# Kernel optimization log

Hardware: AMD Instinct MI355X
Metric: run time of the kernel (lower is better)

Reference implementation:

```python
import jax, jax.numpy as jnp
import numpy as np
from jax import lax

EPS = 1e-5
B, T, H, L, K = 64, 1024, 12, 120, 5  # batch, seq len, hidden, lstm layers, conv kernel


def _init(key, shape, scale):
    return scale * jax.random.normal(key, shape, dtype=jnp.float32)


def setup_inputs() -> dict:
    key = jax.random.key(0)
    ks = jax.random.split(key, 16)
    return {
        "x": jax.random.normal(ks[0], (B, 6, T), dtype=jnp.float32),
        "conv_acc_w": _init(ks[1], (6, 6, K), 0.3),
        "conv_acc_b": jnp.zeros((6,), jnp.float32),
        "bn1_gamma": jnp.ones((6,), jnp.float32),
        "bn1_beta": jnp.zeros((6,), jnp.float32),
        "conv_ang_w": _init(ks[2], (6, 6, K), 0.3),
        "conv_ang_b": jnp.zeros((6,), jnp.float32),
        "bn2_gamma": jnp.ones((6,), jnp.float32),
        "bn2_beta": jnp.zeros((6,), jnp.float32),
        "attn_w": _init(ks[3], (H, 6), 0.4),
        "attn_b": jnp.zeros((H,), jnp.float32),
        "lstm_wih": _init(ks[4], (L, 4 * H, H), 0.2),
        "lstm_whh": _init(ks[5], (L, 4 * H, H), 0.2),
        "lstm_bih": _init(ks[6], (L, 4 * H), 0.1),
        "lstm_bhh": _init(ks[7], (L, 4 * H), 0.1),
        "lin1_w": _init(ks[8], (H, H), 0.3),
        "lin1_b": jnp.zeros((H,), jnp.float32),
        "lin2_w": _init(ks[9], (H, H), 0.3),
        "lin2_b": jnp.zeros((H,), jnp.float32),
        "mu_w": _init(ks[10], (H, H), 0.3),
        "mu_b": jnp.zeros((H,), jnp.float32),
        "sigma_w": _init(ks[11], (H, H), 0.3),
        "sigma_b": jnp.zeros((H,), jnp.float32),
    }


def _conv1d(x, w, b):
    # x: (B, C, T) valid conv, matches nn.Conv1d
    y = lax.conv_general_dilated(x, w, (1,), "VALID", dimension_numbers=("NCH", "OIH", "NCH"))
    return y + b[None, :, None]


def _batchnorm(x, gamma, beta):
    # training-mode BatchNorm1d: biased batch stats over (N, T)
    mean = jnp.mean(x, axis=(0, 2), keepdims=True)
    var = jnp.var(x, axis=(0, 2), keepdims=True)
    return (x - mean) * lax.rsqrt(var + EPS) * gamma[None, :, None] + beta[None, :, None]


def _lstm_stack(seq_tbh, wih, whh, bias):
    # seq_tbh: (T', B, H); stacked 120-layer LSTM, torch gate order (i, f, g, o)
    b = seq_tbh.shape[1]
    h0 = jnp.zeros((b, H), seq_tbh.dtype)

    def layer(seq, p):
        w_ih, w_hh, bb = p

        def step(carry, xt):
            h, c = carry
            g = xt @ w_ih.T + h @ w_hh.T + bb  # (B, 4H)
            i, f, gg, o = jnp.split(g, 4, axis=-1)
            c_new = jax.nn.sigmoid(f) * c + jax.nn.sigmoid(i) * jnp.tanh(gg)
            h_new = jax.nn.sigmoid(o) * jnp.tanh(c_new)
            return (h_new, c_new), h_new

        (h_T, _), out = lax.scan(step, (h0, h0), seq)
        return out, h_T

    _, h_last = lax.scan(layer, seq_tbh, (wih, whh, bias))
    return h_last  # (L, B, H): final hidden state of every layer


def _forward(x, conv_acc_w, conv_acc_b, bn1_gamma, bn1_beta, conv_ang_w, conv_ang_b,
             bn2_gamma, bn2_beta, attn_w, attn_b, lstm_wih, lstm_whh, lstm_bih, lstm_bhh,
             lin1_w, lin1_b, lin2_w, lin2_b, mu_w, mu_b, sigma_w, sigma_b):
    out_acc = jax.nn.relu(_batchnorm(_conv1d(x, conv_acc_w, conv_acc_b), bn1_gamma, bn1_beta))
    out_ang = jax.nn.relu(_batchnorm(_conv1d(out_acc, conv_ang_w, conv_ang_b), bn2_gamma, bn2_beta))
    feat = jax.nn.relu(jnp.einsum("bct,hc->bth", out_ang, attn_w) + attn_b)  # (B, T-8, H)
    seq = jnp.transpose(feat, (1, 0, 2))  # (T', B, H) time-major for scan
    h_last = _lstm_stack(seq, lstm_wih, lstm_whh, lstm_bih + lstm_bhh)
    h = jnp.transpose(h_last, (1, 0, 2))  # (B, L, H) == hidden_state.permute(1,0,2)
    h = jax.nn.relu(h @ lin1_w.T + lin1_b)
    out = jax.nn.relu(h @ lin2_w.T + lin2_b)
    mu = out @ mu_w.T + mu_b
    log_var = jax.nn.softplus(out @ sigma_w.T + sigma_b)
    return out, mu, log_var


def reference(x, conv_acc_w, conv_acc_b, bn1_gamma, bn1_beta, conv_ang_w, conv_ang_b,
              bn2_gamma, bn2_beta, attn_w, attn_b, lstm_wih, lstm_whh, lstm_bih, lstm_bhh,
              lin1_w, lin1_b, lin2_w, lin2_b, mu_w, mu_b, sigma_w, sigma_b):
    return _forward(x, conv_acc_w, conv_acc_b, bn1_gamma, bn1_beta, conv_ang_w, conv_ang_b,
                    bn2_gamma, bn2_beta, attn_w, attn_b, lstm_wih, lstm_whh, lstm_bih, lstm_bhh,
                    lin1_w, lin1_b, lin2_w, lin2_b, mu_w, mu_b, sigma_w, sigma_b)
```

## Files before the change

### kernel.cpp

```cpp
#include <hip/hip_runtime.h>
#include <math.h>

#define NLAY 120
#define TT   1016
#define NB   64
#define RB   8
#define IRS  32
#define TPB  384
#define BIGF (1 << 20)

typedef float v2f __attribute__((ext_vector_type(2)));

__device__ __forceinline__ float fast_rcp(float x) { return __builtin_amdgcn_rcpf(x); }
__device__ __forceinline__ float fast_sig(float x) { return fast_rcp(1.f + __expf(-x)); }
__device__ __forceinline__ float fast_tanh(float x) { return 1.f - 2.f * fast_rcp(1.f + __expf(2.f * x)); }

__device__ __forceinline__ int poll_ge_ag(const int* p, int tgt, int cur) {
  long g = 0;
  while (cur < tgt) {
    cur = __hip_atomic_load(p, __ATOMIC_RELAXED, __HIP_MEMORY_SCOPE_AGENT);
    if (cur >= tgt) break;
    __builtin_amdgcn_s_sleep(1);
    if (++g > 400000L) break;
  }
  return cur;
}
__device__ __forceinline__ int poll_ge_wg(const int* p, int tgt, int cur) {
  long g = 0;
  while (cur < tgt) {
    cur = __hip_atomic_load(p, __ATOMIC_RELAXED, __HIP_MEMORY_SCOPE_WORKGROUP);
    if (cur >= tgt) break;
    __builtin_amdgcn_s_sleep(1);
    if (++g > 400000L) break;
  }
  return cur;
}

__global__ void k_conv(const float* __restrict__ xin, const float* __restrict__ cw,
                       const float* __restrict__ cb, const float* __restrict__ aff,
                       float* __restrict__ yout, float* __restrict__ stat,
                       int Tin, int Tout, int use_aff)
{
  const int bx = blockIdx.x;
  const int b = bx / 6, co = bx - b * 6;
  const int tid = threadIdx.x;
  __shared__ float wsh[30];
  __shared__ float ssh[6], shsh[6];
  if (tid < 30) wsh[tid] = cw[co * 30 + tid];
  if (tid < 6) {
    ssh[tid]  = use_aff ? aff[tid] : 1.f;
    shsh[tid] = use_aff ? aff[6 + tid] : 0.f;
  }
  __syncthreads();
  const float bias = cb[co];
  float lsum = 0.f, lsq = 0.f;
  for (int t = tid; t < Tout; t += 256) {
    float acc = bias;
#pragma unroll
    for (int ci = 0; ci < 6; ++ci) {
      const float* xr = xin + ((size_t)b * 6 + ci) * Tin + t;
      const float s = ssh[ci], sh = shsh[ci];
#pragma unroll
      for (int k = 0; k < 5; ++k) {
        float v = xr[k];
        if (use_aff) v = fmaxf(fmaf(s, v, sh), 0.f);
        acc += wsh[ci * 5 + k] * v;
      }
    }
    yout[((size_t)b * 6 + co) * Tout + t] = acc;
    lsum += acc; lsq += acc * acc;
  }
  __shared__ float rs[256], rq[256];
  rs[tid] = lsum; rq[tid] = lsq;
  __syncthreads();
  for (int s = 128; s > 0; s >>= 1) {
    if (tid < s) { rs[tid] += rs[tid + s]; rq[tid] += rq[tid + s]; }
    __syncthreads();
  }
  if (tid == 0) { atomicAdd(&stat[co], rs[0]); atomicAdd(&stat[6 + co], rq[0]); }
}

__global__ void k_finalize(const float* __restrict__ stat,
                           const float* __restrict__ gamma, const float* __restrict__ beta,
                           float* __restrict__ aff, float invN)
{
  const int c = threadIdx.x;
  if (c < 6) {
    float mean = stat[c] * invN;
    float var  = stat[6 + c] * invN - mean * mean;
    float sc   = gamma[c] * rsqrtf(var + 1e-5f);
    aff[c]     = sc;
    aff[6 + c] = fmaf(-mean, sc, beta[c]);
  }
}

__global__ void k_attn(const float* __restrict__ y2, const float* __restrict__ aff2,
                       const float* __restrict__ aw, const float* __restrict__ ab,
                       float* __restrict__ seq0)
{
  const int t = blockIdx.x;
  const int tid = threadIdx.x;
  __shared__ float zb[6 * 64];
  if (tid < 384) {
    const int c = tid >> 6, bb = tid & 63;
    float v = y2[((size_t)bb * 6 + c) * TT + t];
    zb[c * 64 + bb] = fmaxf(fmaf(aff2[c], v, aff2[6 + c]), 0.f);
  }
  __syncthreads();
  const int b = tid / 12, j = tid - b * 12;
  float acc = ab[j];
#pragma unroll
  for (int c = 0; c < 6; ++c) acc += aw[j * 6 + c] * zb[c * 64 + b];
  seq0[(size_t)t * 768 + tid] = fmaxf(acc, 0.f);
}

__global__ __launch_bounds__(TPB, 2) void k_lstm(
    const float* __restrict__ wih, const float* __restrict__ whh,
    const float* __restrict__ bih, const float* __restrict__ bhh,
    const float* __restrict__ seq0, float* __restrict__ ring,
    int* __restrict__ prog, int* __restrict__ cons,
    float* __restrict__ hfin)
{
  const int bid  = blockIdx.x;
  const int c    = bid >> 2;
  const int seg  = bid & 3;
  const int tid  = threadIdx.x;
  const int w    = tid >> 6;
  const int lane = tid & 63;
  const int p    = lane / 12;
  const int j    = lane - p * 12;
  const bool act = (p < 5);
  const int pc   = act ? p : 0;
  const int l    = seg * 30 + w * 5 + pc;

  __shared__ __align__(16) float hloc[6][2][64];
  __shared__ __align__(16) float iring[5][IRS][12];
  __shared__ __align__(16) float xring[2][16][12];
  __shared__ __align__(16) float oring[16][12];
  __shared__ int pflag[6];
  __shared__ int cflag[8];
  float* xrf = &xring[0][0][0];

  if (tid < 6) pflag[tid] = 0;
  if (tid < 8) cflag[tid] = 0;
  hloc[w][0][lane] = 0.f; hloc[w][1][lane] = 0.f;
  __syncthreads();

  v2f wx_if[12], wx_go[12], wh_if[12], wh_go[12];
  v2f b_if = (v2f){0.f, 0.f}, b_go = (v2f){0.f, 0.f};
  if (act) {
    const float* wi = wih + l * 576;
    const float* wh = whh + l * 576;
#pragma unroll
    for (int k = 0; k < 12; ++k) {
      wx_if[k] = (v2f){ wi[(j     ) * 12 + k], wi[(j + 12) * 12 + k] };
      wx_go[k] = (v2f){ wi[(j + 24) * 12 + k], wi[(j + 36) * 12 + k] };
      wh_if[k] = (v2f){ wh[(j     ) * 12 + k], wh[(j + 12) * 12 + k] };
      wh_go[k] = (v2f){ wh[(j + 24) * 12 + k], wh[(j + 36) * 12 + k] };
    }
    const float* ba = bih + l * 48;
    const float* bb = bhh + l * 48;
    b_if = (v2f){ ba[j]      + bb[j],      ba[j + 12] + bb[j + 12] };
    b_go = (v2f){ ba[j + 24] + bb[j + 24], ba[j + 36] + bb[j + 36] };
  }

  const int hop_in  = c * 3 + seg - 1;
  const int hop_out = c * 3 + seg;
  const float* rin  = ring + (size_t)((seg > 0) ? hop_in : 0) * (RB * 192);
  float*       rout = ring + (size_t)((seg < 3) ? hop_out : 0) * (RB * 192);
  const bool is_feeder = (w == 0);
  const bool is_tailer = (w == 5) && (seg < 3);

  const int f0 = lane, f1 = lane + 64, f2 = lane + 128;
  const int s0o0 = (f0 / 12) * 768 + (f0 % 12);
  const int s0o1 = (f1 / 12) * 768 + (f1 % 12);
  const int s0o2 = (f2 / 12) * 768 + (f2 % 12);

  auto ld_batch = [&](int m, float* d) {
    if (seg == 0) {
      const float* b = seq0 + (size_t)m * 16 * 768 + c * 12;
      d[0] = b[s0o0]; d[1] = b[s0o1]; d[2] = b[s0o2];
    } else {
      const float* b = rin + (m & (RB - 1)) * 192;
      d[0] = __hip_atomic_load(b + f0, __ATOMIC_RELAXED, __HIP_MEMORY_SCOPE_AGENT);
      d[1] = __hip_atomic_load(b + f1, __ATOMIC_RELAXED, __HIP_MEMORY_SCOPE_AGENT);
      d[2] = __hip_atomic_load(b + f2, __ATOMIC_RELAXED, __HIP_MEMORY_SCOPE_AGENT);
    }
  };

  float pend[3] = {0.f, 0.f, 0.f};
  int kp = 0, kcons = 0;
  if (is_feeder) {
    if (seg > 0) kp = poll_ge_ag(&prog[hop_in], 2, 0);
    float cur[3];
    ld_batch(0, cur);
    ld_batch(1, pend);
    xrf[f0] = cur[0]; xrf[f1] = cur[1]; xrf[f2] = cur[2];
  }

  float cst = 0.f;
  int pcache = 0, ccache = 0;

  auto step = [&](int s, bool guard) __attribute__((always_inline)) {
    const int t  = s - pc;
    const int rb = (s & 1) ^ 1, wb = s & 1;

    const float* ax;
    if (p == 0) ax = (w == 0) ? (xrf + ((s >> 4) & 1) * 192 + (s & 15) * 12)
                              : (&iring[w - 1][s & (IRS - 1)][0]);
    else        ax = &hloc[w][rb][(pc == 0 ? 0 : pc - 1) * 12];
    const float* ah = &hloc[w][rb][pc * 12];

    float4 xA = ((const float4*)ax)[0], xB = ((const float4*)ax)[1], xC = ((const float4*)ax)[2];
    float4 hA = ((const float4*)ah)[0], hB = ((const float4*)ah)[1], hC = ((const float4*)ah)[2];
    float xv[12] = {xA.x,xA.y,xA.z,xA.w, xB.x,xB.y,xB.z,xB.w, xC.x,xC.y,xC.z,xC.w};
    float hv[12] = {hA.x,hA.y,hA.z,hA.w, hB.x,hB.y,hB.z,hB.w, hC.x,hC.y,hC.z,hC.w};

    v2f axif = (v2f){0.f,0.f}, axgo = (v2f){0.f,0.f};
    v2f ahif = b_if, ahgo = b_go;
#pragma unroll
    for (int k = 0; k < 12; ++k) {
      v2f xx = { xv[k], xv[k] };
      axif = __builtin_elementwise_fma(wx_if[k], xx, axif);
      axgo = __builtin_elementwise_fma(wx_go[k], xx, axgo);
    }
#pragma unroll
    for (int k = 0; k < 12; ++k) {
      v2f hh = { hv[k], hv[k] };
      ahif = __builtin_elementwise_fma(wh_if[k], hh, ahif);
      ahgo = __builtin_elementwise_fma(wh_go[k], hh, ahgo);
    }
    v2f aif = axif + ahif, ago = axgo + ahgo;
    float ig = fast_sig(aif.x);
    float fg = fast_sig(aif.y);
    float gg = fast_tanh(ago.x);
    float og = fast_sig(ago.y);

    if (!guard) {
      cst = fg * cst + ig * gg;
      float hn = og * fast_tanh(cst);
      hloc[w][wb][p * 12 + j] = hn;
      if (p == 4) {
        if (w < 5) iring[w][t & (IRS - 1)][j] = hn;
        else if (seg < 3) oring[t & 15][j] = hn;
      }
    } else {
      const bool run = act && (t >= 0) && (t < TT);
      if (run) {
        cst = fg * cst + ig * gg;
        float hn = og * fast_tanh(cst);
        hloc[w][wb][p * 12 + j] = hn;
        if (p == 4) {
          if (w < 5) iring[w][t & (IRS - 1)][j] = hn;
          else if (seg < 3) oring[t & 15][j] = hn;
        }
        if (t == TT - 1) hfin[l * 768 + c * 12 + j] = hn;
      }
    }

    if (is_tailer) {
      const int t4 = s - 4;
      if (t4 >= 0 && t4 < TT && (((t4 & 15) == 15) || t4 == TT - 1)) {
        const int m4 = t4 >> 4;
        if (kcons < m4 - (RB - 1) + 1)
          kcons = poll_ge_ag(&cons[hop_out], m4 - RB + 1, kcons);
        const float* orf = &oring[0][0];
        float o0 = orf[f0], o1 = orf[f1], o2 = orf[f2];
        float* d = rout + (m4 & (RB - 1)) * 192;
        __hip_atomic_store(d + f0, o0, __ATOMIC_RELAXED, __HIP_MEMORY_SCOPE_AGENT);
        __hip_atomic_store(d + f1, o1, __ATOMIC_RELAXED, __HIP_MEMORY_SCOPE_AGENT);
        __hip_atomic_store(d + f2, o2, __ATOMIC_RELAXED, __HIP_MEMORY_SCOPE_AGENT);
        if (lane == 0)
          __hip_atomic_store(&prog[hop_out], m4 + 1, __ATOMIC_RELEASE, __HIP_MEMORY_SCOPE_AGENT);
      }
    }
  };

  for (int s4 = 0; s4 < 1024; s4 += 4) {
    if (is_feeder && (s4 & 15) == 0) {
      const int m = s4 >> 4;
      if (m + 1 < NB) {
        float* xd = xrf + ((m + 1) & 1) * 192;
        xd[f0] = pend[0]; xd[f1] = pend[1]; xd[f2] = pend[2];
      }
      if (m + 2 < NB) {
        if (seg > 0 && kp < m + 3) kp = poll_ge_ag(&prog[hop_in], m + 3, kp);
        ld_batch(m + 2, pend);
      }
      if (seg > 0 && lane == 0)
        __hip_atomic_store(&cons[hop_in], m, __ATOMIC_RELAXED, __HIP_MEMORY_SCOPE_AGENT);
    }

    if (w > 0 && s4 < TT) {
      const int tgt = (s4 + 4 < TT) ? (s4 + 4) : TT;
      if (pcache < tgt) {
        pcache = poll_ge_wg(&pflag[w - 1], tgt, pcache);
        asm volatile("" ::: "memory");
      }
    }
    if (w < 5 && s4 >= 36) {
      const int tgt = s4 - 32;
      if (ccache < tgt) {
        ccache = poll_ge_wg(&cflag[w + 1], tgt, ccache);
        asm volatile("" ::: "memory");
      }
    }

    if (s4 >= 4 && s4 < 1012) {
      step(s4 + 0, false); step(s4 + 1, false); step(s4 + 2, false); step(s4 + 3, false);
    } else {
      step(s4 + 0, true);  step(s4 + 1, true);  step(s4 + 2, true);  step(s4 + 3, true);
    }

    if (lane == 0) {
      asm volatile("" ::: "memory");
      if (w < 5)
        __hip_atomic_store(&pflag[w], s4, __ATOMIC_RELAXED, __HIP_MEMORY_SCOPE_WORKGROUP);
      if (w > 0 && s4 + 3 < TT)
        __hip_atomic_store(&cflag[w], s4 + 4, __ATOMIC_RELAXED, __HIP_MEMORY_SCOPE_WORKGROUP);
    }
  }

  if (lane == 0) {
    asm volatile("" ::: "memory");
    if (w < 5) __hip_atomic_store(&pflag[w], BIGF, __ATOMIC_RELAXED, __HIP_MEMORY_SCOPE_WORKGROUP);
    if (w > 0) __hip_atomic_store(&cflag[w], BIGF, __ATOMIC_RELAXED, __HIP_MEMORY_SCOPE_WORKGROUP);
    if (is_feeder && seg > 0)
      __hip_atomic_store(&cons[hop_in], BIGF, __ATOMIC_RELAXED, __HIP_MEMORY_SCOPE_AGENT);
  }
}

__global__ void k_head(const float* __restrict__ hfin,
                       const float* __restrict__ w1, const float* __restrict__ b1,
                       const float* __restrict__ w2, const float* __restrict__ b2,
                       const float* __restrict__ wm, const float* __restrict__ bm,
                       const float* __restrict__ wsg, const float* __restrict__ bsg,
                       float* __restrict__ out)
{
  const int tid = threadIdx.x;
  __shared__ float s1[144], s2[144], sm[144], ss[144];
  __shared__ float v1[12], v2[12], vm[12], vs[12];
  if (tid < 144) { s1[tid] = w1[tid]; s2[tid] = w2[tid]; sm[tid] = wm[tid]; ss[tid] = wsg[tid]; }
  if (tid < 12)  { v1[tid] = b1[tid]; v2[tid] = b2[tid]; vm[tid] = bm[tid]; vs[tid] = bsg[tid]; }
  __syncthreads();
  const int r = blockIdx.x * 256 + tid;
  const int b = r / 120, l = r - b * 120;
  float h[12];
#pragma unroll
  for (int k = 0; k < 12; ++k) h[k] = hfin[l * 768 + b * 12 + k];
  float u1[12];
#pragma unroll
  for (int u = 0; u < 12; ++u) {
    float a = v1[u];
#pragma unroll
    for (int k = 0; k < 12; ++k) a += s1[u * 12 + k] * h[k];
    u1[u] = fmaxf(a, 0.f);
  }
  float u2[12];
#pragma unroll
  for (int u = 0; u < 12; ++u) {
    float a = v2[u];
#pragma unroll
    for (int k = 0; k < 12; ++k) a += s2[u * 12 + k] * u1[k];
    u2[u] = fmaxf(a, 0.f);
  }
  const size_t base = (size_t)r * 12;
#pragma unroll
  for (int u = 0; u < 12; ++u) out[base + u] = u2[u];
#pragma unroll
  for (int u = 0; u < 12; ++u) {
    float a = vm[u];
#pragma unroll
    for (int k = 0; k < 12; ++k) a += sm[u * 12 + k] * u2[k];
    out[92160 + base + u] = a;
  }
#pragma unroll
  for (int u = 0; u < 12; ++u) {
    float a = vs[u];
#pragma unroll
    for (int k = 0; k < 12; ++k) a += ss[u * 12 + k] * u2[k];
    out[184320 + base + u] = fmaxf(a, 0.f) + log1pf(expf(-fabsf(a)));
  }
}

extern "C" void kernel_launch(void* const* d_in, const int* in_sizes, int n_in,
                              void* d_out, int out_size, void* d_ws, size_t ws_size,
                              hipStream_t stream)
{
  const float* x   = (const float*)d_in[0];
  const float* c1w = (const float*)d_in[1];
  const float* c1b = (const float*)d_in[2];
  const float* g1  = (const float*)d_in[3];
  const float* be1 = (const float*)d_in[4];
  const float* c2w = (const float*)d_in[5];
  const float* c2b = (const float*)d_in[6];
  const float* g2  = (const float*)d_in[7];
  const float* be2 = (const float*)d_in[8];
  const float* aw  = (const float*)d_in[9];
  const float* ab  = (const float*)d_in[10];
  const float* wih = (const float*)d_in[11];
  const float* whh = (const float*)d_in[12];
  const float* bih = (const float*)d_in[13];
  const float* bhh = (const float*)d_in[14];
  const float* l1w = (const float*)d_in[15];
  const float* l1b = (const float*)d_in[16];
  const float* l2w = (const float*)d_in[17];
  const float* l2b = (const float*)d_in[18];
  const float* muw = (const float*)d_in[19];
  const float* mub = (const float*)d_in[20];
  const float* sgw = (const float*)d_in[21];
  const float* sgb = (const float*)d_in[22];

  float* ws    = (float*)d_ws;
  float* stat1 = ws;
  float* stat2 = ws + 12;
  float* aff1  = ws + 24;
  float* aff2  = ws + 36;
  int*   prog  = (int*)(ws + 64);
  int*   cons  = (int*)(ws + 304);
  float* y1    = ws + 576;
  float* y2    = y1 + 391680;
  float* seq0  = y2 + 390144;
  float* ring  = seq0 + 780288;
  float* hfin  = ring + (size_t)192 * RB * 192;

  hipMemsetAsync(d_ws, 0, 576 * sizeof(float), stream);

  k_conv<<<384, 256, 0, stream>>>(x, c1w, c1b, nullptr, y1, stat1, 1024, 1020, 0);
  k_finalize<<<1, 64, 0, stream>>>(stat1, g1, be1, aff1, 1.f / 65280.f);
  k_conv<<<384, 256, 0, stream>>>(y1, c2w, c2b, aff1, y2, stat2, 1020, 1016, 1);
  k_finalize<<<1, 64, 0, stream>>>(stat2, g2, be2, aff2, 1.f / 65024.f);
  k_attn<<<1016, 768, 0, stream>>>(y2, aff2, aw, ab, seq0);
  k_lstm<<<256, TPB, 0, stream>>>(wih, whh, bih, bhh, seq0, ring, prog, cons, hfin);
  k_head<<<30, 256, 0, stream>>>(hfin, l1w, l1b, l2w, l2b, muw, mub, sgw, sgb, (float*)d_out);
}
```

Baseline: 812.8 us.

## Exchange LSTM hidden state via ds_bpermute instead of LDS double buffer

Removes the per-wave LDS double buffer for hidden state and instead broadcasts each lane's new h to the next layer lane-group through ds_bpermute cross-lane shuffles, cutting LDS store/load round trips on the serial recurrence path. It also splits the FMA accumulation into two independent chains to shorten dependency latency, switches sigmoid/tanh to raw exp2 intrinsics, drops the s_sleep in the workgroup-scope spin wait, and moves the tailer output flush out of the per-step lambda to once per 4-step block. The risks are more hot spinning on LDS flags and bpermute latency replacing LDS latency.

```diff
diff --git a/kernel.cpp b/kernel.cpp
--- a/kernel.cpp
+++ b/kernel.cpp
@@ -10,10 +10,15 @@
 #define BIGF (1 << 20)
 
 typedef float v2f __attribute__((ext_vector_type(2)));
+typedef float v4f __attribute__((ext_vector_type(4)));
 
 __device__ __forceinline__ float fast_rcp(float x) { return __builtin_amdgcn_rcpf(x); }
-__device__ __forceinline__ float fast_sig(float x) { return fast_rcp(1.f + __expf(-x)); }
-__device__ __forceinline__ float fast_tanh(float x) { return 1.f - 2.f * fast_rcp(1.f + __expf(2.f * x)); }
+__device__ __forceinline__ float sigx(float x) {
+  return fast_rcp(1.f + __builtin_amdgcn_exp2f(-1.442695040888963f * x));
+}
+__device__ __forceinline__ float tanhx(float x) {
+  return 1.f - 2.f * fast_rcp(1.f + __builtin_amdgcn_exp2f(2.885390081777927f * x));
+}
 
 __device__ __forceinline__ int poll_ge_ag(const int* p, int tgt, int cur) {
   long g = 0;
@@ -30,8 +35,7 @@
   while (cur < tgt) {
     cur = __hip_atomic_load(p, __ATOMIC_RELAXED, __HIP_MEMORY_SCOPE_WORKGROUP);
     if (cur >= tgt) break;
-    __builtin_amdgcn_s_sleep(1);
-    if (++g > 400000L) break;
+    if (++g > 3000000L) break;
   }
   return cur;
 }
@@ -131,9 +135,11 @@
   const int j    = lane - p * 12;
   const bool act = (p < 5);
   const int pc   = act ? p : 0;
+  const int pp   = (pc == 0) ? 0 : pc - 1;
   const int l    = seg * 30 + w * 5 + pc;
-
-  __shared__ __align__(16) float hloc[6][2][64];
+  const int base_own = pc * 48;
+  const int base_prv = pp * 48;
+
   __shared__ __align__(16) float iring[5][IRS][12];
   __shared__ __align__(16) float xring[2][16][12];
   __shared__ __align__(16) float oring[16][12];
@@ -143,7 +149,6 @@
 
   if (tid < 6) pflag[tid] = 0;
   if (tid < 8) cflag[tid] = 0;
-  hloc[w][0][lane] = 0.f; hloc[w][1][lane] = 0.f;
   __syncthreads();
 
   v2f wx_if[12], wx_go[12], wh_if[12], wh_go[12];
@@ -198,48 +203,60 @@
     xrf[f0] = cur[0]; xrf[f1] = cur[1]; xrf[f2] = cur[2];
   }
 
-  float cst = 0.f;
+  float hn = 0.f, cst = 0.f;
   int pcache = 0, ccache = 0;
 
   auto step = [&](int s, bool guard) __attribute__((always_inline)) {
     const int t  = s - pc;
-    const int rb = (s & 1) ^ 1, wb = s & 1;
-
-    const float* ax;
-    if (p == 0) ax = (w == 0) ? (xrf + ((s >> 4) & 1) * 192 + (s & 15) * 12)
-                              : (&iring[w - 1][s & (IRS - 1)][0]);
-    else        ax = &hloc[w][rb][(pc == 0 ? 0 : pc - 1) * 12];
-    const float* ah = &hloc[w][rb][pc * 12];
-
-    float4 xA = ((const float4*)ax)[0], xB = ((const float4*)ax)[1], xC = ((const float4*)ax)[2];
-    float4 hA = ((const float4*)ah)[0], hB = ((const float4*)ah)[1], hC = ((const float4*)ah)[2];
-    float xv[12] = {xA.x,xA.y,xA.z,xA.w, xB.x,xB.y,xB.z,xB.w, xC.x,xC.y,xC.z,xC.w};
-    float hv[12] = {hA.x,hA.y,hA.z,hA.w, hB.x,hB.y,hB.z,hB.w, hC.x,hC.y,hC.z,hC.w};
-
-    v2f axif = (v2f){0.f,0.f}, axgo = (v2f){0.f,0.f};
-    v2f ahif = b_if, ahgo = b_go;
-#pragma unroll
-    for (int k = 0; k < 12; ++k) {
-      v2f xx = { xv[k], xv[k] };
-      axif = __builtin_elementwise_fma(wx_if[k], xx, axif);
-      axgo = __builtin_elementwise_fma(wx_go[k], xx, axgo);
-    }
-#pragma unroll
-    for (int k = 0; k < 12; ++k) {
-      v2f hh = { hv[k], hv[k] };
-      ahif = __builtin_elementwise_fma(wh_if[k], hh, ahif);
-      ahgo = __builtin_elementwise_fma(wh_go[k], hh, ahgo);
-    }
-    v2f aif = axif + ahif, ago = axgo + ahgo;
-    float ig = fast_sig(aif.x);
-    float fg = fast_sig(aif.y);
-    float gg = fast_tanh(ago.x);
-    float og = fast_sig(ago.y);
+    const int hb = __float_as_int(hn);
+
+    float hv[12], xv[12];
+#pragma unroll
+    for (int k = 0; k < 12; ++k)
+      hv[k] = __int_as_float(__builtin_amdgcn_ds_bpermute(base_own + 4 * k, hb));
+#pragma unroll
+    for (int k = 0; k < 12; ++k)
+      xv[k] = __int_as_float(__builtin_amdgcn_ds_bpermute(base_prv + 4 * k, hb));
+
+    if (p == 0) {
+      const float* ax = (w == 0) ? (xrf + ((s >> 4) & 1) * 192 + (s & 15) * 12)
+                                 : (&iring[w - 1][s & (IRS - 1)][0]);
+      v4f A = ((const v4f*)ax)[0], Bv = ((const v4f*)ax)[1], C = ((const v4f*)ax)[2];
+      xv[0] = A.x;  xv[1] = A.y;  xv[2]  = A.z;  xv[3]  = A.w;
+      xv[4] = Bv.x; xv[5] = Bv.y; xv[6]  = Bv.z; xv[7]  = Bv.w;
+      xv[8] = C.x;  xv[9] = C.y;  xv[10] = C.z;  xv[11] = C.w;
+    }
+
+    v2f xia = b_if, xib = (v2f){0.f, 0.f};
+    v2f xga = b_go, xgb = (v2f){0.f, 0.f};
+    v2f hia = (v2f){0.f, 0.f}, hib = (v2f){0.f, 0.f};
+    v2f hga = (v2f){0.f, 0.f}, hgb = (v2f){0.f, 0.f};
+#pragma unroll
+    for (int k = 0; k < 6; ++k) {
+      v2f xs = (v2f){ xv[k], xv[k] }, hs = (v2f){ hv[k], hv[k] };
+      xia = __builtin_elementwise_fma(wx_if[k], xs, xia);
+      xga = __builtin_elementwise_fma(wx_go[k], xs, xga);
+      hia = __builtin_elementwise_fma(wh_if[k], hs, hia);
+      hga = __builtin_elementwise_fma(wh_go[k], hs, hga);
+    }
+#pragma unroll
+    for (int k = 6; k < 12; ++k) {
+      v2f xs = (v2f){ xv[k], xv[k] }, hs = (v2f){ hv[k], hv[k] };
+      xib = __builtin_elementwise_fma(wx_if[k], xs, xib);
+      xgb = __builtin_elementwise_fma(wx_go[k], xs, xgb);
+      hib = __builtin_elementwise_fma(wh_if[k], hs, hib);
+      hgb = __builtin_elementwise_fma(wh_go[k], hs, hgb);
+    }
+    v2f aif = (xia + xib) + (hia + hib);
+    v2f ago = (xga + xgb) + (hga + hgb);
+    float ig = sigx(aif.x);
+    float fg = sigx(aif.y);
+    float gg = tanhx(ago.x);
+    float og = sigx(ago.y);
 
     if (!guard) {
       cst = fg * cst + ig * gg;
-      float hn = og * fast_tanh(cst);
-      hloc[w][wb][p * 12 + j] = hn;
+      hn = og * tanhx(cst);
       if (p == 4) {
         if (w < 5) iring[w][t & (IRS - 1)][j] = hn;
         else if (seg < 3) oring[t & 15][j] = hn;
@@ -248,8 +265,7 @@
       const bool run = act && (t >= 0) && (t < TT);
       if (run) {
         cst = fg * cst + ig * gg;
-        float hn = og * fast_tanh(cst);
-        hloc[w][wb][p * 12 + j] = hn;
+        hn = og * tanhx(cst);
         if (p == 4) {
           if (w < 5) iring[w][t & (IRS - 1)][j] = hn;
           else if (seg < 3) oring[t & 15][j] = hn;
@@ -257,11 +273,47 @@
         if (t == TT - 1) hfin[l * 768 + c * 12 + j] = hn;
       }
     }
+  };
+
+  for (int s4 = 0; s4 < 1024; s4 += 4) {
+    if (is_feeder && (s4 & 15) == 0) {
+      const int m = s4 >> 4;
+      if (m + 1 < NB) {
+        float* xd = xrf + ((m + 1) & 1) * 192;
+        xd[f0] = pend[0]; xd[f1] = pend[1]; xd[f2] = pend[2];
+      }
+      if (m + 2 < NB) {
+        if (seg > 0 && kp < m + 3) kp = poll_ge_ag(&prog[hop_in], m + 3, kp);
+        ld_batch(m + 2, pend);
+      }
+      if (seg > 0 && lane == 0)
+        __hip_atomic_store(&cons[hop_in], m, __ATOMIC_RELAXED, __HIP_MEMORY_SCOPE_AGENT);
+    }
+
+    if (w > 0 && s4 < TT) {
+      const int tgt = (s4 + 4 < TT) ? (s4 + 4) : TT;
+      if (pcache < tgt) {
+        pcache = poll_ge_wg(&pflag[w - 1], tgt, pcache);
+        asm volatile("" ::: "memory");
+      }
+    }
+    if (w < 5 && s4 >= 36) {
+      const int tgt = s4 - 32;
+      if (ccache < tgt) {
+        ccache = poll_ge_wg(&cflag[w + 1], tgt, ccache);
+        asm volatile("" ::: "memory");
+      }
+    }
+
+    if (s4 >= 4 && s4 < 1012) {
+      step(s4 + 0, false); step(s4 + 1, false); step(s4 + 2, false); step(s4 + 3, false);
+    } else {
+      step(s4 + 0, true);  step(s4 + 1, true);  step(s4 + 2, true);  step(s4 + 3, true);
+    }
 
     if (is_tailer) {
-      const int t4 = s - 4;
-      if (t4 >= 0 && t4 < TT && (((t4 & 15) == 15) || t4 == TT - 1)) {
-        const int m4 = t4 >> 4;
+      if ((((s4 & 15) == 0) && s4 >= 16) || s4 == 1016) {
+        const int m4 = (s4 - 1) >> 4;
         if (kcons < m4 - (RB - 1) + 1)
           kcons = poll_ge_ag(&cons[hop_out], m4 - RB + 1, kcons);
         const float* orf = &oring[0][0];
@@ -273,43 +325,6 @@
         if (lane == 0)
           __hip_atomic_store(&prog[hop_out], m4 + 1, __ATOMIC_RELEASE, __HIP_MEMORY_SCOPE_AGENT);
       }
-    }
-  };
-
-  for (int s4 = 0; s4 < 1024; s4 += 4) {
-    if (is_feeder && (s4 & 15) == 0) {
-      const int m = s4 >> 4;
-      if (m + 1 < NB) {
-        float* xd = xrf + ((m + 1) & 1) * 192;
-        xd[f0] = pend[0]; xd[f1] = pend[1]; xd[f2] = pend[2];
-      }
-      if (m + 2 < NB) {
-        if (seg > 0 && kp < m + 3) kp = poll_ge_ag(&prog[hop_in], m + 3, kp);
-        ld_batch(m + 2, pend);
-      }
-      if (seg > 0 && lane == 0)
-        __hip_atomic_store(&cons[hop_in], m, __ATOMIC_RELAXED, __HIP_MEMORY_SCOPE_AGENT);
-    }
-
-    if (w > 0 && s4 < TT) {
-      const int tgt = (s4 + 4 < TT) ? (s4 + 4) : TT;
-      if (pcache < tgt) {
-        pcache = poll_ge_wg(&pflag[w - 1], tgt, pcache);
-        asm volatile("" ::: "memory");
-      }
-    }
-    if (w < 5 && s4 >= 36) {
-      const int tgt = s4 - 32;
-      if (ccache < tgt) {
-        ccache = poll_ge_wg(&cflag[w + 1], tgt, ccache);
-        asm volatile("" ::: "memory");
-      }
-    }
-
-    if (s4 >= 4 && s4 < 1012) {
-      step(s4 + 0, false); step(s4 + 1, false); step(s4 + 2, false); step(s4 + 3, false);
-    } else {
-      step(s4 + 0, true);  step(s4 + 1, true);  step(s4 + 2, true);  step(s4 + 3, true);
     }
 
     if (lane == 0) {
```

After: 986.0 us. +21.3%, slower.

## Process two batch columns per LSTM block, halving block count

Applied to the files above, without the earlier changes.

Each LSTM workgroup now carries two batch elements through the layer pipeline instead of one. The per-thread weights held in registers are reused for both columns, and all shared-memory rings and the global hop rings are doubled in width, so the grid shrinks from 256 to 128 blocks. The tailer flush that pushes outputs to the next segment moves out of the per-step lambda into the 4-step loop body, so it is checked once per group of four steps rather than on every step. This gives each wave twice the independent FMA and transcendental work between synchronisation points, at the cost of more register pressure and fewer blocks spread across the CUs.

```diff
diff --git a/kernel.cpp b/kernel.cpp
--- a/kernel.cpp
+++ b/kernel.cpp
@@ -122,7 +122,7 @@
     float* __restrict__ hfin)
 {
   const int bid  = blockIdx.x;
-  const int c    = bid >> 2;
+  const int pr   = bid >> 2;
   const int seg  = bid & 3;
   const int tid  = threadIdx.x;
   const int w    = tid >> 6;
@@ -133,17 +133,20 @@
   const int pc   = act ? p : 0;
   const int l    = seg * 30 + w * 5 + pc;
 
-  __shared__ __align__(16) float hloc[6][2][64];
-  __shared__ __align__(16) float iring[5][IRS][12];
-  __shared__ __align__(16) float xring[2][16][12];
-  __shared__ __align__(16) float oring[16][12];
+  __shared__ __align__(16) float hloc[6][2][2][64];
+  __shared__ __align__(16) float iring[5][IRS][2][12];
+  __shared__ __align__(16) float xring[2][16][2][12];
+  __shared__ __align__(16) float oring[16][2][12];
   __shared__ int pflag[6];
   __shared__ int cflag[8];
-  float* xrf = &xring[0][0][0];
+  float* xrf = &xring[0][0][0][0];
 
   if (tid < 6) pflag[tid] = 0;
   if (tid < 8) cflag[tid] = 0;
-  hloc[w][0][lane] = 0.f; hloc[w][1][lane] = 0.f;
+#pragma unroll
+  for (int z = 0; z < 2; ++z) {
+    hloc[w][0][z][lane] = 0.f; hloc[w][1][z][lane] = 0.f;
+  }
   __syncthreads();
 
   v2f wx_if[12], wx_go[12], wh_if[12], wh_go[12];
@@ -164,114 +167,140 @@
     b_go = (v2f){ ba[j + 24] + bb[j + 24], ba[j + 36] + bb[j + 36] };
   }
 
-  const int hop_in  = c * 3 + seg - 1;
-  const int hop_out = c * 3 + seg;
-  const float* rin  = ring + (size_t)((seg > 0) ? hop_in : 0) * (RB * 192);
-  float*       rout = ring + (size_t)((seg < 3) ? hop_out : 0) * (RB * 192);
+  const int hop_in  = pr * 3 + seg - 1;
+  const int hop_out = pr * 3 + seg;
+  const float* rin  = ring + (size_t)((seg > 0) ? hop_in : 0) * (RB * 384);
+  float*       rout = ring + (size_t)((seg < 3) ? hop_out : 0) * (RB * 384);
   const bool is_feeder = (w == 0);
   const bool is_tailer = (w == 5) && (seg < 3);
 
-  const int f0 = lane, f1 = lane + 64, f2 = lane + 128;
-  const int s0o0 = (f0 / 12) * 768 + (f0 % 12);
-  const int s0o1 = (f1 / 12) * 768 + (f1 % 12);
-  const int s0o2 = (f2 / 12) * 768 + (f2 % 12);
+  int s0o[6];
+#pragma unroll
+  for (int k = 0; k < 6; ++k) {
+    const int fk = lane + 64 * k;
+    const int tl = fk / 24, rem = fk - tl * 24;
+    const int ch = rem / 12, jj = rem - ch * 12;
+    s0o[k] = tl * 768 + ch * 12 + jj;
+  }
 
   auto ld_batch = [&](int m, float* d) {
     if (seg == 0) {
-      const float* b = seq0 + (size_t)m * 16 * 768 + c * 12;
-      d[0] = b[s0o0]; d[1] = b[s0o1]; d[2] = b[s0o2];
+      const float* b = seq0 + (size_t)m * 16 * 768 + pr * 24;
+#pragma unroll
+      for (int k = 0; k < 6; ++k) d[k] = b[s0o[k]];
     } else {
-      const float* b = rin + (m & (RB - 1)) * 192;
-      d[0] = __hip_atomic_load(b + f0, __ATOMIC_RELAXED, __HIP_MEMORY_SCOPE_AGENT);
-      d[1] = __hip_atomic_load(b + f1, __ATOMIC_RELAXED, __HIP_MEMORY_SCOPE_AGENT);
-      d[2] = __hip_atomic_load(b + f2, __ATOMIC_RELAXED, __HIP_MEMORY_SCOPE_AGENT);
+      const float* b = rin + (m & (RB - 1)) * 384;
+#pragma unroll
+      for (int k = 0; k < 6; ++k)
+        d[k] = __hip_atomic_load(b + lane + 64 * k, __ATOMIC_RELAXED, __HIP_MEMORY_SCOPE_AGENT);
     }
   };
 
-  float pend[3] = {0.f, 0.f, 0.f};
+  float pend[6] = {0.f, 0.f, 0.f, 0.f, 0.f, 0.f};
   int kp = 0, kcons = 0;
   if (is_feeder) {
     if (seg > 0) kp = poll_ge_ag(&prog[hop_in], 2, 0);
-    float cur[3];
+    float cur[6];
     ld_batch(0, cur);
     ld_batch(1, pend);
-    xrf[f0] = cur[0]; xrf[f1] = cur[1]; xrf[f2] = cur[2];
-  }
-
-  float cst = 0.f;
+#pragma unroll
+    for (int k = 0; k < 6; ++k) xrf[lane + 64 * k] = cur[k];
+  }
+
+  float cstA = 0.f, cstB = 0.f;
   int pcache = 0, ccache = 0;
 
   auto step = [&](int s, bool guard) __attribute__((always_inline)) {
     const int t  = s - pc;
     const int rb = (s & 1) ^ 1, wb = s & 1;
 
-    const float* ax;
-    if (p == 0) ax = (w == 0) ? (xrf + ((s >> 4) & 1) * 192 + (s & 15) * 12)
-                              : (&iring[w - 1][s & (IRS - 1)][0]);
-    else        ax = &hloc[w][rb][(pc == 0 ? 0 : pc - 1) * 12];
-    const float* ah = &hloc[w][rb][pc * 12];
-
-    float4 xA = ((const float4*)ax)[0], xB = ((const float4*)ax)[1], xC = ((const float4*)ax)[2];
-    float4 hA = ((const float4*)ah)[0], hB = ((const float4*)ah)[1], hC = ((const float4*)ah)[2];
-    float xv[12] = {xA.x,xA.y,xA.z,xA.w, xB.x,xB.y,xB.z,xB.w, xC.x,xC.y,xC.z,xC.w};
-    float hv[12] = {hA.x,hA.y,hA.z,hA.w, hB.x,hB.y,hB.z,hB.w, hC.x,hC.y,hC.z,hC.w};
-
-    v2f axif = (v2f){0.f,0.f}, axgo = (v2f){0.f,0.f};
-    v2f ahif = b_if, ahgo = b_go;
+    const float *axA, *axB;
+    if (p == 0) {
+      if (w == 0) {
+        float* base = xrf + ((s >> 4) & 1) * 384 + (s & 15) * 24;
+        axA = base; axB = base + 12;
+      } else {
+        axA = &iring[w - 1][s & (IRS - 1)][0][0];
+        axB = &iring[w - 1][s & (IRS - 1)][1][0];
+      }
+    } else {
+      axA = &hloc[w][rb][0][(pc == 0 ? 0 : pc - 1) * 12];
+      axB = &hloc[w][rb][1][(pc == 0 ? 0 : pc - 1) * 12];
+    }
+    const float* ahA = &hloc[w][rb][0][pc * 12];
+    const float* ahB = &hloc[w][rb][1][pc * 12];
+
+    float4 xA0 = ((const float4*)axA)[0], xA1 = ((const float4*)axA)[1], xA2 = ((const float4*)axA)[2];
+    float4 hA0 = ((const float4*)ahA)[0], hA1 = ((const float4*)ahA)[1], hA2 = ((const float4*)ahA)[2];
+    float4 xB0 = ((const float4*)axB)[0], xB1 = ((const float4*)axB)[1], xB2 = ((const float4*)axB)[2];
+    float4 hB0 = ((const float4*)ahB)[0], hB1 = ((const float4*)ahB)[1], hB2 = ((const float4*)ahB)[2];
+    float xvA[12] = {xA0.x,xA0.y,xA0.z,xA0.w, xA1.x,xA1.y,xA1.z,xA1.w, xA2.x,xA2.y,xA2.z,xA2.w};
+    float hvA[12] = {hA0.x,hA0.y,hA0.z,hA0.w, hA1.x,hA1.y,hA1.z,hA1.w, hA2.x,hA2.y,hA2.z,hA2.w};
+    float xvB[12] = {xB0.x,xB0.y,xB0.z,xB0.w, xB1.x,xB1.y,xB1.z,xB1.w, xB2.x,xB2.y,xB2.z,xB2.w};
+    float hvB[12] = {hB0.x,hB0.y,hB0.z,hB0.w, hB1.x,hB1.y,hB1.z,hB1.w, hB2.x,hB2.y,hB2.z,hB2.w};
+
+    v2f axifA = (v2f){0.f,0.f}, axgoA = (v2f){0.f,0.f};
+    v2f ahifA = b_if, ahgoA = b_go;
+    v2f axifB = (v2f){0.f,0.f}, axgoB = (v2f){0.f,0.f};
+    v2f ahifB = b_if, ahgoB = b_go;
 #pragma unroll
     for (int k = 0; k < 12; ++k) {
-      v2f xx = { xv[k], xv[k] };
-      axif = __builtin_elementwise_fma(wx_if[k], xx, axif);
-      axgo = __builtin_elementwise_fma(wx_go[k], xx, axgo);
-    }
-#pragma unroll
-    for (int k = 0; k < 12; ++k) {
-      v2f hh = { hv[k], hv[k] };
-      ahif = __builtin_elementwise_fma(wh_if[k], hh, ahif);
-      ahgo = __builtin_elementwise_fma(wh_go[k], hh, ahgo);
-    }
-    v2f aif = axif + ahif, ago = axgo + ahgo;
-    float ig = fast_sig(aif.x);
-    float fg = fast_sig(aif.y);
-    float gg = fast_tanh(ago.x);
-    float og = fast_sig(ago.y);
+      v2f xxA = { xvA[k], xvA[k] }, hhA = { hvA[k], hvA[k] };
+      v2f xxB = { xvB[k], xvB[k] }, hhB = { hvB[k], hvB[k] };
+      axifA = __builtin_elementwise_fma(wx_if[k], xxA, axifA);
+      axgoA = __builtin_elementwise_fma(wx_go[k], xxA, axgoA);
+      ahifA = __builtin_elementwise_fma(wh_if[k], hhA, ahifA);
+      ahgoA = __builtin_elementwise_fma(wh_go[k], hhA, ahgoA);
+      axifB = __builtin_elementwise_fma(wx_if[k], xxB, axifB);
+      axgoB = __builtin_elementwise_fma(wx_go[k], xxB, axgoB);
+      ahifB = __builtin_elementwise_fma(wh_if[k], hhB, ahifB);
+      ahgoB = __builtin_elementwise_fma(wh_go[k], hhB, ahgoB);
+    }
+    v2f aifA = axifA + ahifA, agoA = axgoA + ahgoA;
+    v2f aifB = axifB + ahifB, agoB = axgoB + ahgoB;
+    float igA = fast_sig(aifA.x), fgA = fast_sig(aifA.y);
+    float ggA = fast_tanh(agoA.x), ogA = fast_sig(agoA.y);
+    float igB = fast_sig(aifB.x), fgB = fast_sig(aifB.y);
+    float ggB = fast_tanh(agoB.x), ogB = fast_sig(agoB.y);
 
     if (!guard) {
-      cst = fg * cst + ig * gg;
-      float hn = og * fast_tanh(cst);
-      hloc[w][wb][p * 12 + j] = hn;
+      cstA = fgA * cstA + igA * ggA;
+      cstB = fgB * cstB + igB * ggB;
+      float hnA = ogA * fast_tanh(cstA);
+      float hnB = ogB * fast_tanh(cstB);
+      hloc[w][wb][0][p * 12 + j] = hnA;
+      hloc[w][wb][1][p * 12 + j] = hnB;
       if (p == 4) {
-        if (w < 5) iring[w][t & (IRS - 1)][j] = hn;
-        else if (seg < 3) oring[t & 15][j] = hn;
+        if (w < 5) {
+          iring[w][t & (IRS - 1)][0][j] = hnA;
+          iring[w][t & (IRS - 1)][1][j] = hnB;
+        } else if (seg < 3) {
+          oring[t & 15][0][j] = hnA;
+          oring[t & 15][1][j] = hnB;
+        }
       }
     } else {
       const bool run = act && (t >= 0) && (t < TT);
       if (run) {
-        cst = fg * cst + ig * gg;
-        float hn = og * fast_tanh(cst);
-        hloc[w][wb][p * 12 + j] = hn;
+        cstA = fgA * cstA + igA * ggA;
+        cstB = fgB * cstB + igB * ggB;
+        float hnA = ogA * fast_tanh(cstA);
+        float hnB = ogB * fast_tanh(cstB);
+        hloc[w][wb][0][p * 12 + j] = hnA;
+        hloc[w][wb][1][p * 12 + j] = hnB;
         if (p == 4) {
-          if (w < 5) iring[w][t & (IRS - 1)][j] = hn;
-          else if (seg < 3) oring[t & 15][j] = hn;
+          if (w < 5) {
+            iring[w][t & (IRS - 1)][0][j] = hnA;
+            iring[w][t & (IRS - 1)][1][j] = hnB;
+          } else if (seg < 3) {
+            oring[t & 15][0][j] = hnA;
+            oring[t & 15][1][j] = hnB;
+          }
         }
-        if (t == TT - 1) hfin[l * 768 + c * 12 + j] = hn;
-      }
-    }
-
-    if (is_tailer) {
-      const int t4 = s - 4;
-      if (t4 >= 0 && t4 < TT && (((t4 & 15) == 15) || t4 == TT - 1)) {
-        const int m4 = t4 >> 4;
-        if (kcons < m4 - (RB - 1) + 1)
-          kcons = poll_ge_ag(&cons[hop_out], m4 - RB + 1, kcons);
-        const float* orf = &oring[0][0];
-        float o0 = orf[f0], o1 = orf[f1], o2 = orf[f2];
-        float* d = rout + (m4 & (RB - 1)) * 192;
-        __hip_atomic_store(d + f0, o0, __ATOMIC_RELAXED, __HIP_MEMORY_SCOPE_AGENT);
-        __hip_atomic_store(d + f1, o1, __ATOMIC_RELAXED, __HIP_MEMORY_SCOPE_AGENT);
-        __hip_atomic_store(d + f2, o2, __ATOMIC_RELAXED, __HIP_MEMORY_SCOPE_AGENT);
-        if (lane == 0)
-          __hip_atomic_store(&prog[hop_out], m4 + 1, __ATOMIC_RELEASE, __HIP_MEMORY_SCOPE_AGENT);
+        if (t == TT - 1) {
+          hfin[l * 768 + (2 * pr)     * 12 + j] = hnA;
+          hfin[l * 768 + (2 * pr + 1) * 12 + j] = hnB;
+        }
       }
     }
   };
@@ -280,8 +309,9 @@
     if (is_feeder && (s4 & 15) == 0) {
       const int m = s4 >> 4;
       if (m + 1 < NB) {
-        float* xd = xrf + ((m + 1) & 1) * 192;
-        xd[f0] = pend[0]; xd[f1] = pend[1]; xd[f2] = pend[2];
+        float* xd = xrf + ((m + 1) & 1) * 384;
+#pragma unroll
+        for (int k = 0; k < 6; ++k) xd[lane + 64 * k] = pend[k];
       }
       if (m + 2 < NB) {
         if (seg > 0 && kp < m + 3) kp = poll_ge_ag(&prog[hop_in], m + 3, kp);
@@ -310,6 +340,24 @@
       step(s4 + 0, false); step(s4 + 1, false); step(s4 + 2, false); step(s4 + 3, false);
     } else {
       step(s4 + 0, true);  step(s4 + 1, true);  step(s4 + 2, true);  step(s4 + 3, true);
+    }
+
+    if (is_tailer) {
+      if ((((s4 & 15) == 0) && s4 >= 16) || s4 == 1016) {
+        const int m4 = (s4 - 1) >> 4;
+        if (kcons < m4 - (RB - 1) + 1)
+          kcons = poll_ge_ag(&cons[hop_out], m4 - RB + 1, kcons);
+        const float* orf = &oring[0][0][0];
+        float o[6];
+#pragma unroll
+        for (int k = 0; k < 6; ++k) o[k] = orf[lane + 64 * k];
+        float* d = rout + (m4 & (RB - 1)) * 384;
+#pragma unroll
+        for (int k = 0; k < 6; ++k)
+          __hip_atomic_store(d + lane + 64 * k, o[k], __ATOMIC_RELAXED, __HIP_MEMORY_SCOPE_AGENT);
+        if (lane == 0)
+          __hip_atomic_store(&prog[hop_out], m4 + 1, __ATOMIC_RELEASE, __HIP_MEMORY_SCOPE_AGENT);
+      }
     }
 
     if (lane == 0) {
@@ -422,7 +470,7 @@
   float* y2    = y1 + 391680;
   float* seq0  = y2 + 390144;
   float* ring  = seq0 + 780288;
-  float* hfin  = ring + (size_t)192 * RB * 192;
+  float* hfin  = ring + (size_t)96 * RB * 384;
 
   hipMemsetAsync(d_ws, 0, 576 * sizeof(float), stream);
 
@@ -431,6 +479,6 @@
   k_conv<<<384, 256, 0, stream>>>(y1, c2w, c2b, aff1, y2, stat2, 1020, 1016, 1);
   k_finalize<<<1, 64, 0, stream>>>(stat2, g2, be2, aff2, 1.f / 65024.f);
   k_attn<<<1016, 768, 0, stream>>>(y2, aff2, aw, ab, seq0);
-  k_lstm<<<256, TPB, 0, stream>>>(wih, whh, bih, bhh, seq0, ring, prog, cons, hfin);
+  k_lstm<<<128, TPB, 0, stream>>>(wih, whh, bih, bhh, seq0, ring, prog, cons, hfin);
   k_head<<<30, 256, 0, stream>>>(hfin, l1w, l1b, l2w, l2b, muw, mub, sgw, sgb, (float*)d_out);
 }
```

Measured after the change: 1.334 ms. 64.1% more time.
